# Kernel optimization log

Measured on AMD Instinct MI355X. Metric: run time of the kernel, lower is better.

The kernel has to match this reference:

```python
import jax, jax.numpy as jnp
import numpy as np


def _lstm(x, Wk, Wr, b, reverse, return_seq):
    # Keras LSTM with activation='relu', recurrent_activation='sigmoid'.
    # Wk: (F, 4H), Wr: (H, 4H), b: (4H). Gate order: i, f, c, o.
    if reverse:
        x = jnp.flip(x, 1)
    H = Wr.shape[0]
    xg = jnp.einsum('btf,fg->btg', x, Wk) + b  # (B, T, 4H)
    B = x.shape[0]

    def step(carry, g_t):
        h, c = carry
        g = g_t + h @ Wr
        i = jax.nn.sigmoid(g[:, :H])
        f = jax.nn.sigmoid(g[:, H:2 * H])
        cc = jax.nn.relu(g[:, 2 * H:3 * H])
        o = jax.nn.sigmoid(g[:, 3 * H:])
        c = f * c + i * cc
        h = o * jax.nn.relu(c)
        return (h, c), h

    init = (jnp.zeros((B, H), x.dtype), jnp.zeros((B, H), x.dtype))
    (h, _), hs = jax.lax.scan(step, init, jnp.swapaxes(xg, 0, 1))
    if return_seq:
        hs = jnp.swapaxes(hs, 0, 1)  # (B, T, H)
        if reverse:
            hs = jnp.flip(hs, 1)
        return hs
    return h


def setup_inputs() -> dict:
    key = jax.random.key(0)
    ks = jax.random.split(key, 24)
    B, LA, T, F = 256, 200, 512, 128
    s = 0.05
    d = {
        'inputA': jax.random.randint(ks[0], (B, LA), 0, 1000),
        'inputB': jax.random.normal(ks[1], (B, T, F), jnp.float32),
        'emb': jax.random.normal(ks[2], (1000, 3), jnp.float32) * s,
        'w1': jax.random.normal(ks[3], (600, 256), jnp.float32) * s,
        'b1': jnp.zeros((256,), jnp.float32),
        'w2': jax.random.normal(ks[4], (256, 128), jnp.float32) * s,
        'b2': jnp.zeros((128,), jnp.float32),
        'w3': jax.random.normal(ks[5], (128, 64), jnp.float32) * s,
        'b3': jnp.zeros((64,), jnp.float32),
        'k1f': jax.random.normal(ks[6], (128, 512), jnp.float32) * s,
        'r1f': jax.random.normal(ks[7], (128, 512), jnp.float32) * s,
        'bb1f': jnp.zeros((512,), jnp.float32),
        'k1b': jax.random.normal(ks[8], (128, 512), jnp.float32) * s,
        'r1b': jax.random.normal(ks[9], (128, 512), jnp.float32) * s,
        'bb1b': jnp.zeros((512,), jnp.float32),
        'k2f': jax.random.normal(ks[10], (256, 256), jnp.float32) * s,
        'r2f': jax.random.normal(ks[11], (64, 256), jnp.float32) * s,
        'bb2f': jnp.zeros((256,), jnp.float32),
        'k2b': jax.random.normal(ks[12], (256, 256), jnp.float32) * s,
        'r2b': jax.random.normal(ks[13], (64, 256), jnp.float32) * s,
        'bb2b': jnp.zeros((256,), jnp.float32),
        'wz1': jax.random.normal(ks[14], (192, 2), jnp.float32) * s,
        'bz1': jnp.zeros((2,), jnp.float32),
        'wz2': jax.random.normal(ks[15], (2, 1), jnp.float32) * s,
        'bz2': jnp.zeros((1,), jnp.float32),
        'wt1': jax.random.normal(ks[16], (192, 2), jnp.float32) * s,
        'bt1': jnp.zeros((2,), jnp.float32),
        'wt2': jax.random.normal(ks[17], (2, 1), jnp.float32) * s,
        'bt2': jnp.zeros((1,), jnp.float32),
    }
    return d


def reference(inputA, inputB, emb, w1, b1, w2, b2, w3, b3,
              k1f, r1f, bb1f, k1b, r1b, bb1b,
              k2f, r2f, bb2f, k2b, r2b, bb2b,
              wz1, bz1, wz2, bz2, wt1, bt1, wt2, bt2):
    B = inputA.shape[0]
    # Embedding branch
    x = emb[inputA]                       # (B, LA, 3)
    x = x.reshape(B, -1)                  # flatten -> (B, 600)
    x = jax.nn.relu(x @ w1 + b1)
    x = jax.nn.relu(x @ w2 + b2)
    x = jax.nn.relu(x @ w3 + b3)          # (B, 64)
    # BiLSTM branch
    y_f = _lstm(inputB, k1f, r1f, bb1f, reverse=False, return_seq=True)
    y_b = _lstm(inputB, k1b, r1b, bb1b, reverse=True, return_seq=True)
    y = jnp.concatenate([y_f, y_b], axis=-1)   # (B, T, 256)
    h_f = _lstm(y, k2f, r2f, bb2f, reverse=False, return_seq=False)
    h_b = _lstm(y, k2b, r2b, bb2b, reverse=True, return_seq=False)
    y = jnp.concatenate([h_f, h_b], axis=-1)    # (B, 128)
    combined = jnp.concatenate([x, y], axis=-1)  # (B, 192)
    z = jax.nn.relu(combined @ wz1 + bz1) @ wz2 + bz2
    t = jax.nn.relu(combined @ wt1 + bt1) @ wt2 + bt2
    return (z, t)
```

## Files before the change

kernel.cpp:

```cpp
#include <hip/hip_runtime.h>

typedef __attribute__((ext_vector_type(8))) short s8v;
typedef __attribute__((ext_vector_type(4))) short s4v;
typedef __attribute__((ext_vector_type(4))) float f4v;

#if __has_builtin(__builtin_amdgcn_exp2f)
#define EXP2(x) __builtin_amdgcn_exp2f(x)
#else
#define EXP2(x) exp2f(x)
#endif
#if __has_builtin(__builtin_amdgcn_rcpf)
#define RCP(x) __builtin_amdgcn_rcpf(x)
#else
#define RCP(x) (1.0f/(x))
#endif

#define LOG2E 1.4426950408889634f

__device__ __forceinline__ short f2bf(float f) {
    union { float f; unsigned u; } x; x.f = f;
    unsigned r = (x.u + 0x7FFFu + ((x.u >> 16) & 1u)) >> 16;
    return (short)r;
}
__device__ __forceinline__ float bf2f(short s) {
    union { unsigned u; float f; } x; x.u = ((unsigned)(unsigned short)s) << 16;
    return x.f;
}
__device__ __forceinline__ void lds_barrier() {
    asm volatile("s_waitcnt lgkmcnt(0)\n\ts_barrier" ::: "memory");
}

__global__ __launch_bounds__(256) void prep_embed_kernel(
        const float* __restrict__ k1f, const float* __restrict__ r1f,
        const float* __restrict__ k1b, const float* __restrict__ r1b,
        const float* __restrict__ k2f, const float* __restrict__ r2f,
        const float* __restrict__ k2b, const float* __restrict__ r2b,
        short* __restrict__ WB1, short* __restrict__ WB2,
        const int* __restrict__ inputA, const float* __restrict__ emb,
        const float* __restrict__ w1, const float* __restrict__ b1,
        const float* __restrict__ w2, const float* __restrict__ b2,
        const float* __restrict__ w3, const float* __restrict__ b3,
        float* __restrict__ xe) {
    if (blockIdx.x < 1024) {
        int idx = blockIdx.x * 256 + threadIdx.x;
        if (idx < 262144) {
            int j = idx & 7, l = (idx >> 3) & 63, c = (idx >> 9) & 7, n = (idx >> 12) & 31, d = (idx >> 17) & 1;
            int coln = n * 16 + (l & 15);
            int k = c * 32 + ((l >> 4) * 8) + j;
            const float* Wk = d ? k1b : k1f;
            const float* Wr = d ? r1b : r1f;
            float v = (c < 4) ? Wk[k * 512 + coln] : Wr[(k - 128) * 512 + coln];
            float sc = ((n >> 3) == 2) ? 1.0f : -LOG2E;
            WB1[idx] = f2bf(v * sc);
        }
        if (idx < 163840) {
            int d = idx / 81920, r0 = idx % 81920;
            int n = r0 / 5120, r1 = r0 % 5120;
            int c = r1 / 512, li = r1 % 512;
            int l = li >> 3, j = li & 7;
            int coln = n * 16 + (l & 15);
            int k = c * 32 + ((l >> 4) * 8) + j;
            const float* Wk = d ? k2b : k2f;
            const float* Wr = d ? r2b : r2f;
            float v = (k < 256) ? Wk[k * 256 + coln] : Wr[(k - 256) * 256 + coln];
            float sc = ((n >> 2) == 2) ? 1.0f : -LOG2E;
            WB2[idx] = f2bf(v * sc);
        }
        return;
    }
    __shared__ float row[600];
    __shared__ float h1[256];
    __shared__ float h2[128];
    int b = blockIdx.x - 1024, t = threadIdx.x;
    if (t < 200) {
        int idx = inputA[b * 200 + t];
        row[t * 3 + 0] = emb[idx * 3 + 0];
        row[t * 3 + 1] = emb[idx * 3 + 1];
        row[t * 3 + 2] = emb[idx * 3 + 2];
    }
    __syncthreads();
    float a = b1[t];
    for (int k = 0; k < 600; k++) a += row[k] * w1[k * 256 + t];
    h1[t] = fmaxf(a, 0.f);
    __syncthreads();
    if (t < 128) {
        float a2 = b2[t];
        for (int k = 0; k < 256; k++) a2 += h1[k] * w2[k * 128 + t];
        h2[t] = fmaxf(a2, 0.f);
    }
    __syncthreads();
    if (t < 64) {
        float a3 = b3[t];
        for (int k = 0; k < 128; k++) a3 += h2[k] * w3[k * 64 + t];
        xe[b * 64 + t] = fmaxf(a3, 0.f);
    }
}

__global__ __launch_bounds__(512, 2) void megastep(
        const float* __restrict__ x, const short* __restrict__ WB1, const short* __restrict__ WB2,
        const float* __restrict__ bb1f, const float* __restrict__ bb1b,
        const float* __restrict__ bb2f, const float* __restrict__ bb2b,
        short* __restrict__ yfr, short* __restrict__ xgA, short* __restrict__ xgB,
        short* __restrict__ ygA, short* __restrict__ ygB,
        float* __restrict__ c1st, short* __restrict__ h1st,
        float* __restrict__ c2st, short* __restrict__ h2st,
        float* __restrict__ h2o, int k, int TC, int NC) {
    __shared__ short hA[2048];
    __shared__ short hB[2048];
    __shared__ short stg[38912];
    const int tid = threadIdx.x, lane = tid & 63, w = tid >> 6;
    const int bid = blockIdx.x;
    const int tgn = TC >> 3;

    if (bid < 32) {
        const int cl = k - 1;
        if (cl < 0 || cl >= NC) return;
        const int t0 = cl * TC;
        const int first = (cl == 0);
        const int btile = bid & 15, dir = bid >> 4;
        const int col = lane & 15, q = lane >> 4, u = (w << 4) + col;
        const int sb = dir * 16 + btile;

        s8v wf[4][4];
#pragma unroll
        for (int ti = 0; ti < 4; ti++)
#pragma unroll
            for (int c = 0; c < 4; c++)
                wf[ti][c] = *(const s8v*)(WB1 + ((((dir * 32 + (w + 8 * ti)) * 8) + 4 + c) * 64 + lane) * 8);

        float cst[4], hl[4];
        if (first) {
#pragma unroll
            for (int r = 0; r < 4; r++) cst[r] = 0.f;
            for (int i = tid; i < 2048; i += 512) hA[i] = 0;
        } else {
            f4v cv = *(const f4v*)(c1st + ((size_t)sb * 8 + w) * 256 + lane * 4);
#pragma unroll
            for (int r = 0; r < 4; r++) cst[r] = cv[r];
            for (int i = tid; i < 2048; i += 512) hA[i] = h1st[sb * 2048 + i];
        }
        __syncthreads();

        const short* xgp = ((cl & 1) ? xgB : xgA) + (size_t)sb * TC * 8192 + w * 1024 + lane * 8;
        s8v pe0 = *(const s8v*)(xgp);
        s8v pe1 = *(const s8v*)(xgp + 512);
        s8v po0 = *(const s8v*)(xgp + 8192);
        s8v po1 = *(const s8v*)(xgp + 8192 + 512);

        const int hidx = (w >> 1) * 512 + ((u >> 3) & 3) * 128 + (u & 7);

        for (int s = 0; s < TC; s += 2) {
            {
                s8v ah[4];
#pragma unroll
                for (int cc = 0; cc < 4; cc++) ah[cc] = *(const s8v*)&hA[(cc * 64 + lane) * 8];
                if (w >= 4 && s > 0) {
                    int tp = t0 + s - 1;
                    if (dir) tp = 511 - tp;
                    s8v hv = (w == 4) ? ah[0] : (w == 5) ? ah[1] : (w == 6) ? ah[2] : ah[3];
                    *(s8v*)(yfr + (((size_t)(btile * 512 + tp) * 8) + dir * 4 + (w - 4)) * 512 + lane * 8) = hv;
                }
                f4v acc[4];
#pragma unroll
                for (int r = 0; r < 4; r++) {
                    acc[0][r] = bf2f(pe0[r]);
                    acc[1][r] = bf2f(pe0[4 + r]);
                    acc[2][r] = bf2f(pe1[r]);
                    acc[3][r] = bf2f(pe1[4 + r]);
                }
                {
                    const short* np = xgp + (size_t)(s + 2) * 8192;
                    pe0 = *(const s8v*)np;
                    pe1 = *(const s8v*)(np + 512);
                }
#pragma unroll
                for (int cc = 0; cc < 4; cc++)
#pragma unroll
                    for (int ti = 0; ti < 4; ti++)
                        acc[ti] = __builtin_amdgcn_mfma_f32_16x16x32_bf16(ah[cc], wf[ti][cc], acc[ti], 0, 0, 0);
#pragma unroll
                for (int r = 0; r < 4; r++) {
                    float iv = RCP(1.0f + EXP2(acc[0][r]));
                    float fv = RCP(1.0f + EXP2(acc[1][r]));
                    float ov = RCP(1.0f + EXP2(acc[3][r]));
                    float ccv = fmaxf(acc[2][r], 0.f);
                    cst[r] = fv * cst[r] + iv * ccv;
                    hl[r] = ov * fmaxf(cst[r], 0.f);
                }
#pragma unroll
                for (int r = 0; r < 4; r++)
                    hB[hidx + ((q * 4 + r) << 3)] = f2bf(hl[r]);
                lds_barrier();
            }
            {
                s8v ah[4];
#pragma unroll
                for (int cc = 0; cc < 4; cc++) ah[cc] = *(const s8v*)&hB[(cc * 64 + lane) * 8];
                if (w >= 4) {
                    int tp = t0 + s;
                    if (dir) tp = 511 - tp;
                    s8v hv = (w == 4) ? ah[0] : (w == 5) ? ah[1] : (w == 6) ? ah[2] : ah[3];
                    *(s8v*)(yfr + (((size_t)(btile * 512 + tp) * 8) + dir * 4 + (w - 4)) * 512 + lane * 8) = hv;
                }
                f4v acc[4];
#pragma unroll
                for (int r = 0; r < 4; r++) {
                    acc[0][r] = bf2f(po0[r]);
                    acc[1][r] = bf2f(po0[4 + r]);
                    acc[2][r] = bf2f(po1[r]);
                    acc[3][r] = bf2f(po1[4 + r]);
                }
                {
                    const short* np = xgp + (size_t)(s + 3) * 8192;
                    po0 = *(const s8v*)np;
                    po1 = *(const s8v*)(np + 512);
                }
#pragma unroll
                for (int cc = 0; cc < 4; cc++)
#pragma unroll
                    for (int ti = 0; ti < 4; ti++)
                        acc[ti] = __builtin_amdgcn_mfma_f32_16x16x32_bf16(ah[cc], wf[ti][cc], acc[ti], 0, 0, 0);
#pragma unroll
                for (int r = 0; r < 4; r++) {
                    float iv = RCP(1.0f + EXP2(acc[0][r]));
                    float fv = RCP(1.0f + EXP2(acc[1][r]));
                    float ov = RCP(1.0f + EXP2(acc[3][r]));
                    float ccv = fmaxf(acc[2][r], 0.f);
                    cst[r] = fv * cst[r] + iv * ccv;
                    hl[r] = ov * fmaxf(cst[r], 0.f);
                }
#pragma unroll
                for (int r = 0; r < 4; r++)
                    hA[hidx + ((q * 4 + r) << 3)] = f2bf(hl[r]);
                lds_barrier();
            }
        }
        if (w >= 4) {
            int tp = t0 + TC - 1;
            if (dir) tp = 511 - tp;
            s8v hv = *(const s8v*)&hA[((w - 4) * 64 + lane) * 8];
            *(s8v*)(yfr + (((size_t)(btile * 512 + tp) * 8) + dir * 4 + (w - 4)) * 512 + lane * 8) = hv;
        }
        f4v cv;
#pragma unroll
        for (int r = 0; r < 4; r++) cv[r] = cst[r];
        *(f4v*)(c1st + ((size_t)sb * 8 + w) * 256 + lane * 4) = cv;
        for (int i = tid; i < 2048; i += 512) h1st[sb * 2048 + i] = hA[i];
        return;
    }

    if (bid < 64) {
        const int c2 = k - 3;
        if (c2 < 0 || c2 >= NC) return;
        const int first = (c2 == 0), last = (c2 == NC - 1);
        const int btile = (bid - 32) & 15, dir = (bid - 32) >> 4;
        const int b0 = btile << 4;
        const int w4 = w & 3;
        const int col = lane & 15, q = lane >> 4, u = (w4 << 4) + col;
        const int sb = dir * 16 + btile;

        s8v wf[4][2];
#pragma unroll
        for (int ti = 0; ti < 4; ti++)
#pragma unroll
            for (int c = 0; c < 2; c++)
                wf[ti][c] = *(const s8v*)(WB2 + ((((dir * 16 + (w4 + 4 * ti)) * 10) + 8 + c) * 64 + lane) * 8);

        float cst[4], hl[4] = {0.f, 0.f, 0.f, 0.f};
        if (first) {
#pragma unroll
            for (int r = 0; r < 4; r++) cst[r] = 0.f;
            for (int i = tid; i < 1024; i += 512) hA[i] = 0;
        } else {
            f4v cv = *(const f4v*)(c2st + ((size_t)sb * 4 + w4) * 256 + lane * 4);
#pragma unroll
            for (int r = 0; r < 4; r++) cst[r] = cv[r];
            for (int i = tid; i < 1024; i += 512) hA[i] = h2st[sb * 1024 + i];
        }
        __syncthreads();

        const short* ygp = ((c2 & 1) ? ygB : ygA) + (size_t)sb * TC * 4096 + w4 * 1024 + lane * 8;
        s8v pe0, pe1, po0, po1;
        if (w < 4) {
            pe0 = *(const s8v*)(ygp);
            pe1 = *(const s8v*)(ygp + 512);
            po0 = *(const s8v*)(ygp + 4096);
            po1 = *(const s8v*)(ygp + 4096 + 512);
        }
        const int hidx = (w4 >> 1) * 512 + ((u >> 3) & 3) * 128 + (u & 7);

        for (int s = 0; s < TC; s += 2) {
            if (w < 4) {
                s8v ah[2];
#pragma unroll
                for (int cc = 0; cc < 2; cc++) ah[cc] = *(const s8v*)&hA[(cc * 64 + lane) * 8];
                f4v acc[4];
#pragma unroll
                for (int r = 0; r < 4; r++) {
                    acc[0][r] = bf2f(pe0[r]);
                    acc[1][r] = bf2f(pe0[4 + r]);
                    acc[2][r] = bf2f(pe1[r]);
                    acc[3][r] = bf2f(pe1[4 + r]);
                }
                {
                    const short* np = ygp + (size_t)(s + 2) * 4096;
                    pe0 = *(const s8v*)np;
                    pe1 = *(const s8v*)(np + 512);
                }
#pragma unroll
                for (int cc = 0; cc < 2; cc++)
#pragma unroll
                    for (int ti = 0; ti < 4; ti++)
                        acc[ti] = __builtin_amdgcn_mfma_f32_16x16x32_bf16(ah[cc], wf[ti][cc], acc[ti], 0, 0, 0);
#pragma unroll
                for (int r = 0; r < 4; r++) {
                    float iv = RCP(1.0f + EXP2(acc[0][r]));
                    float fv = RCP(1.0f + EXP2(acc[1][r]));
                    float ov = RCP(1.0f + EXP2(acc[3][r]));
                    float ccv = fmaxf(acc[2][r], 0.f);
                    cst[r] = fv * cst[r] + iv * ccv;
                    hl[r] = ov * fmaxf(cst[r], 0.f);
                }
#pragma unroll
                for (int r = 0; r < 4; r++)
                    hB[hidx + ((q * 4 + r) << 3)] = f2bf(hl[r]);
            }
            lds_barrier();
            if (w < 4) {
                s8v ah[2];
#pragma unroll
                for (int cc = 0; cc < 2; cc++) ah[cc] = *(const s8v*)&hB[(cc * 64 + lane) * 8];
                f4v acc[4];
#pragma unroll
                for (int r = 0; r < 4; r++) {
                    acc[0][r] = bf2f(po0[r]);
                    acc[1][r] = bf2f(po0[4 + r]);
                    acc[2][r] = bf2f(po1[r]);
                    acc[3][r] = bf2f(po1[4 + r]);
                }
                {
                    const short* np = ygp + (size_t)(s + 3) * 4096;
                    po0 = *(const s8v*)np;
                    po1 = *(const s8v*)(np + 512);
                }
#pragma unroll
                for (int cc = 0; cc < 2; cc++)
#pragma unroll
                    for (int ti = 0; ti < 4; ti++)
                        acc[ti] = __builtin_amdgcn_mfma_f32_16x16x32_bf16(ah[cc], wf[ti][cc], acc[ti], 0, 0, 0);
#pragma unroll
                for (int r = 0; r < 4; r++) {
                    float iv = RCP(1.0f + EXP2(acc[0][r]));
                    float fv = RCP(1.0f + EXP2(acc[1][r]));
                    float ov = RCP(1.0f + EXP2(acc[3][r]));
                    float ccv = fmaxf(acc[2][r], 0.f);
                    cst[r] = fv * cst[r] + iv * ccv;
                    hl[r] = ov * fmaxf(cst[r], 0.f);
                }
#pragma unroll
                for (int r = 0; r < 4; r++)
                    hA[hidx + ((q * 4 + r) << 3)] = f2bf(hl[r]);
            }
            lds_barrier();
        }
        if (w < 4) {
            f4v cv;
#pragma unroll
            for (int r = 0; r < 4; r++) cv[r] = cst[r];
            *(f4v*)(c2st + ((size_t)sb * 4 + w4) * 256 + lane * 4) = cv;
        }
        __syncthreads();
        for (int i = tid; i < 1024; i += 512) h2st[sb * 1024 + i] = hA[i];
        if (last && w < 4) {
#pragma unroll
            for (int r = 0; r < 4; r++)
                h2o[((dir * 256) + b0 + q * 4 + r) * 64 + u] = hl[r];
        }
        return;
    }

    if (bid < 64 + 4 * TC) {
        const int cg = k;
        if (cg >= NC) return;
        const int t0 = cg * TC;
        const int g = bid - 64;
        const int btile = g & 15;
        const int rest = g >> 4;
        const int tg = rest % tgn;
        const int dir = rest / tgn;
        const int b0 = btile << 4;
        short* xg_w = (cg & 1) ? xgB : xgA;
        {
            int tglob = t0 + tg * 8 + w;
            if (dir) tglob = 511 - tglob;
            const int half = lane >> 5;
            const int f0 = (lane & 31) * 4;
            const int cx = f0 >> 5, qq = (f0 >> 3) & 3, j0 = f0 & 7;
#pragma unroll
            for (int rr = 0; rr < 8; rr++) {
                const int m = rr * 2 + half;
                const float* xp = x + ((size_t)(b0 + m) * 512 + tglob) * 128 + f0;
                f4v v4 = *(const f4v*)xp;
                const int slot = (qq << 4) | ((m ^ qq ^ (cx << 1)) & 15);
                s4v pk;
#pragma unroll
                for (int j = 0; j < 4; j++) pk[j] = f2bf(v4[j]);
                *(s4v*)&stg[(((w * 4 + cx) * 64 + slot) * 8) + j0] = pk;
            }
        }
        s8v wf[4][4];
#pragma unroll
        for (int ti = 0; ti < 4; ti++)
#pragma unroll
            for (int c = 0; c < 4; c++)
                wf[ti][c] = *(const s8v*)(WB1 + ((((dir * 32 + (w + 8 * ti)) * 8) + c) * 64 + lane) * 8);
        const float* bb = dir ? bb1b : bb1f;
        float bias[4];
#pragma unroll
        for (int ti = 0; ti < 4; ti++) {
            const int tile = w + 8 * ti;
            float sc = ((tile >> 3) == 2) ? 1.0f : -LOG2E;
            bias[ti] = sc * bb[tile * 16 + (lane & 15)];
        }
        __syncthreads();
        const size_t sb = dir * 16 + btile;
#pragma unroll 2
        for (int sl = 0; sl < 8; sl++) {
            s8v a[4];
#pragma unroll
            for (int c = 0; c < 4; c++) {
                const int slot = lane ^ (lane >> 4) ^ (c << 1);
                a[c] = *(const s8v*)&stg[((sl * 4 + c) * 64 + slot) * 8];
            }
            f4v acc[4];
#pragma unroll
            for (int ti = 0; ti < 4; ti++) { f4v z = {0.f, 0.f, 0.f, 0.f}; acc[ti] = z; }
#pragma unroll
            for (int c = 0; c < 4; c++)
#pragma unroll
                for (int ti = 0; ti < 4; ti++)
                    acc[ti] = __builtin_amdgcn_mfma_f32_16x16x32_bf16(a[c], wf[ti][c], acc[ti], 0, 0, 0);
            short* outp = xg_w + ((sb * TC + (size_t)(tg * 8 + sl)) * 8 + w) * 1024 + lane * 8;
#pragma unroll
            for (int p = 0; p < 2; p++) {
                s8v v;
#pragma unroll
                for (int j = 0; j < 4; j++) {
                    v[j]     = f2bf(acc[2 * p][j]     + bias[2 * p]);
                    v[4 + j] = f2bf(acc[2 * p + 1][j] + bias[2 * p + 1]);
                }
                *(s8v*)(outp + p * 512) = v;
            }
        }
        return;
    }

    {
        const int cg = k - 2;
        if (cg < 0 || cg >= NC) return;
        const int t0 = cg * TC;
        const int g = bid - 64 - 4 * TC;
        const int btile = g & 15;
        const int rest = g >> 4;
        const int tg = rest % tgn;
        const int dir = rest / tgn;
        short* yg_w = (cg & 1) ? ygB : ygA;
        const int w4 = w & 3, sh = (w >> 2) * 4;
        s8v wf[4][8];
#pragma unroll
        for (int ti = 0; ti < 4; ti++)
#pragma unroll
            for (int c = 0; c < 8; c++)
                wf[ti][c] = *(const s8v*)(WB2 + ((((dir * 16 + (w4 + 4 * ti)) * 10) + c) * 64 + lane) * 8);
        const float* bb = dir ? bb2b : bb2f;
        float bias[4];
#pragma unroll
        for (int ti = 0; ti < 4; ti++) {
            const int tile = w4 + 4 * ti;
            float sc = ((tile >> 2) == 2) ? 1.0f : -LOG2E;
            bias[ti] = sc * bb[tile * 16 + (lane & 15)];
        }
        const size_t sb = dir * 16 + btile;
#pragma unroll
        for (int si = 0; si < 4; si++) {
            const int sl = sh + si;
            int tglob = t0 + tg * 8 + sl;
            if (dir) tglob = 511 - tglob;
            s8v a[8];
#pragma unroll
            for (int c = 0; c < 8; c++)
                a[c] = *(const s8v*)(yfr + (((size_t)(btile * 512 + tglob) * 8) + c) * 512 + lane * 8);
            f4v acc[4];
#pragma unroll
            for (int ti = 0; ti < 4; ti++) { f4v z = {0.f, 0.f, 0.f, 0.f}; acc[ti] = z; }
#pragma unroll
            for (int c = 0; c < 8; c++)
#pragma unroll
                for (int ti = 0; ti < 4; ti++)
                    acc[ti] = __builtin_amdgcn_mfma_f32_16x16x32_bf16(a[c], wf[ti][c], acc[ti], 0, 0, 0);
            short* outp = yg_w + ((sb * TC + (size_t)(tg * 8 + sl)) * 4 + w4) * 1024 + lane * 8;
#pragma unroll
            for (int p = 0; p < 2; p++) {
                s8v v;
#pragma unroll
                for (int j = 0; j < 4; j++) {
                    v[j]     = f2bf(acc[2 * p][j]     + bias[2 * p]);
                    v[4 + j] = f2bf(acc[2 * p + 1][j] + bias[2 * p + 1]);
                }
                *(s8v*)(outp + p * 512) = v;
            }
        }
    }
}

__global__ void heads_kernel(const float* __restrict__ xe, const float* __restrict__ h2o,
                             const float* __restrict__ wz1, const float* __restrict__ bz1,
                             const float* __restrict__ wz2, const float* __restrict__ bz2,
                             const float* __restrict__ wt1, const float* __restrict__ bt1,
                             const float* __restrict__ wt2, const float* __restrict__ bt2,
                             float* __restrict__ out) {
    int b = threadIdx.x;
    float cz0 = bz1[0], cz1 = bz1[1], ct0 = bt1[0], ct1 = bt1[1];
    for (int k = 0; k < 192; k++) {
        float v = (k < 64) ? xe[b * 64 + k]
                : (k < 128) ? h2o[b * 64 + (k - 64)]
                            : h2o[(256 + b) * 64 + (k - 128)];
        cz0 += v * wz1[k * 2 + 0];
        cz1 += v * wz1[k * 2 + 1];
        ct0 += v * wt1[k * 2 + 0];
        ct1 += v * wt1[k * 2 + 1];
    }
    cz0 = fmaxf(cz0, 0.f); cz1 = fmaxf(cz1, 0.f);
    ct0 = fmaxf(ct0, 0.f); ct1 = fmaxf(ct1, 0.f);
    out[b] = cz0 * wz2[0] + cz1 * wz2[1] + bz2[0];
    out[256 + b] = ct0 * wt2[0] + ct1 * wt2[1] + bt2[0];
}

extern "C" void kernel_launch(void* const* d_in, const int* in_sizes, int n_in,
                              void* d_out, int out_size, void* d_ws, size_t ws_size,
                              hipStream_t stream) {
    const int*   inputA = (const int*)d_in[0];
    const float* inputB = (const float*)d_in[1];
    const float* emb = (const float*)d_in[2];
    const float* w1  = (const float*)d_in[3];
    const float* b1  = (const float*)d_in[4];
    const float* w2  = (const float*)d_in[5];
    const float* b2  = (const float*)d_in[6];
    const float* w3  = (const float*)d_in[7];
    const float* b3  = (const float*)d_in[8];
    const float* k1f = (const float*)d_in[9];
    const float* r1f = (const float*)d_in[10];
    const float* bb1f= (const float*)d_in[11];
    const float* k1b = (const float*)d_in[12];
    const float* r1b = (const float*)d_in[13];
    const float* bb1b= (const float*)d_in[14];
    const float* k2f = (const float*)d_in[15];
    const float* r2f = (const float*)d_in[16];
    const float* bb2f= (const float*)d_in[17];
    const float* k2b = (const float*)d_in[18];
    const float* r2b = (const float*)d_in[19];
    const float* bb2b= (const float*)d_in[20];
    const float* wz1 = (const float*)d_in[21];
    const float* bz1 = (const float*)d_in[22];
    const float* wz2 = (const float*)d_in[23];
    const float* bz2 = (const float*)d_in[24];
    const float* wt1 = (const float*)d_in[25];
    const float* bt1 = (const float*)d_in[26];
    const float* wt2 = (const float*)d_in[27];
    const float* bt2 = (const float*)d_in[28];

    char* ws = (char*)d_ws;
    short* WB1  = (short*)(ws);
    short* WB2  = (short*)(ws + 524288);
    float* xe   = (float*)(ws + 851968);
    float* h2o  = (float*)(ws + 917504);
    float* c1st = (float*)(ws + 1048576);
    short* h1st = (short*)(ws + 1310720);
    float* c2st = (float*)(ws + 1441792);
    short* h2st = (short*)(ws + 1572864);
    short* yfr  = (short*)(ws + 2097152);
    float* out  = (float*)d_out;

    int TC = 32;
    if (69206016ull + 2ull * 64 * 524288 + 2ull * 64 * 262144 + 65536 <= ws_size) TC = 64;
    const int NC = 512 / TC;
    short* xgA = (short*)(ws + 69206016);
    short* xgB = xgA + (size_t)TC * 262144;
    short* ygA = xgB + (size_t)TC * 262144;
    short* ygB = ygA + (size_t)TC * 131072;
    const int grid = 64 + 8 * TC;

    prep_embed_kernel<<<1280, 256, 0, stream>>>(k1f, r1f, k1b, r1b, k2f, r2f, k2b, r2b,
                                                WB1, WB2, inputA, emb, w1, b1, w2, b2, w3, b3, xe);
    for (int k = 0; k < NC + 3; k++) {
        megastep<<<grid, 512, 0, stream>>>(inputB, WB1, WB2, bb1f, bb1b, bb2f, bb2b,
                                           yfr, xgA, xgB, ygA, ygB,
                                           c1st, h1st, c2st, h2st, h2o, k, TC, NC);
    }
    heads_kernel<<<1, 256, 0, stream>>>(xe, h2o, wz1, bz1, wz2, bz2, wt1, bt1, wt2, bt2, out);
}
```

Before: 673.4 us.

## Fuse layer-2 input projection into recurrent block via LDS ring, drop yg buffers

```diff
diff --git a/kernel.cpp b/kernel.cpp
--- a/kernel.cpp
+++ b/kernel.cpp
@@ -3,6 +3,7 @@
 typedef __attribute__((ext_vector_type(8))) short s8v;
 typedef __attribute__((ext_vector_type(4))) short s4v;
 typedef __attribute__((ext_vector_type(4))) float f4v;
+typedef __attribute__((ext_vector_type(4))) unsigned u4v;
 
 #if __has_builtin(__builtin_amdgcn_exp2f)
 #define EXP2(x) __builtin_amdgcn_exp2f(x)
@@ -22,9 +23,16 @@
     unsigned r = (x.u + 0x7FFFu + ((x.u >> 16) & 1u)) >> 16;
     return (short)r;
 }
-__device__ __forceinline__ float bf2f(short s) {
-    union { unsigned u; float f; } x; x.u = ((unsigned)(unsigned short)s) << 16;
-    return x.f;
+__device__ __forceinline__ float bflo(unsigned u) {
+    union { unsigned u; float f; } x; x.u = u << 16; return x.f;
+}
+__device__ __forceinline__ float bfhi(unsigned u) {
+    union { unsigned u; float f; } x; x.u = u & 0xffff0000u; return x.f;
+}
+__device__ __forceinline__ unsigned cvt_pk_bf16(float lo, float hi) {
+    unsigned r;
+    asm("v_cvt_pk_bf16_f32 %0, %1, %2" : "=v"(r) : "v"(lo), "v"(hi));
+    return r;
 }
 __device__ __forceinline__ void lds_barrier() {
     asm volatile("s_waitcnt lgkmcnt(0)\n\ts_barrier" ::: "memory");
@@ -101,13 +109,12 @@
         const float* __restrict__ bb1f, const float* __restrict__ bb1b,
         const float* __restrict__ bb2f, const float* __restrict__ bb2b,
         short* __restrict__ yfr, short* __restrict__ xgA, short* __restrict__ xgB,
-        short* __restrict__ ygA, short* __restrict__ ygB,
         float* __restrict__ c1st, short* __restrict__ h1st,
         float* __restrict__ c2st, short* __restrict__ h2st,
         float* __restrict__ h2o, int k, int TC, int NC) {
     __shared__ short hA[2048];
     __shared__ short hB[2048];
-    __shared__ short stg[38912];
+    __shared__ __align__(16) short stg[38912];
     const int tid = threadIdx.x, lane = tid & 63, w = tid >> 6;
     const int bid = blockIdx.x;
     const int tgn = TC >> 3;
@@ -128,7 +135,7 @@
             for (int c = 0; c < 4; c++)
                 wf[ti][c] = *(const s8v*)(WB1 + ((((dir * 32 + (w + 8 * ti)) * 8) + 4 + c) * 64 + lane) * 8);
 
-        float cst[4], hl[4];
+        float cst[4];
         if (first) {
 #pragma unroll
             for (int r = 0; r < 4; r++) cst[r] = 0.f;
@@ -142,10 +149,10 @@
         __syncthreads();
 
         const short* xgp = ((cl & 1) ? xgB : xgA) + (size_t)sb * TC * 8192 + w * 1024 + lane * 8;
-        s8v pe0 = *(const s8v*)(xgp);
-        s8v pe1 = *(const s8v*)(xgp + 512);
-        s8v po0 = *(const s8v*)(xgp + 8192);
-        s8v po1 = *(const s8v*)(xgp + 8192 + 512);
+        u4v pe0 = *(const u4v*)(xgp);
+        u4v pe1 = *(const u4v*)(xgp + 512);
+        u4v po0 = *(const u4v*)(xgp + 8192);
+        u4v po1 = *(const u4v*)(xgp + 8192 + 512);
 
         const int hidx = (w >> 1) * 512 + ((u >> 3) & 3) * 128 + (u & 7);
 
@@ -161,35 +168,37 @@
                     *(s8v*)(yfr + (((size_t)(btile * 512 + tp) * 8) + dir * 4 + (w - 4)) * 512 + lane * 8) = hv;
                 }
                 f4v acc[4];
-#pragma unroll
-                for (int r = 0; r < 4; r++) {
-                    acc[0][r] = bf2f(pe0[r]);
-                    acc[1][r] = bf2f(pe0[4 + r]);
-                    acc[2][r] = bf2f(pe1[r]);
-                    acc[3][r] = bf2f(pe1[4 + r]);
-                }
+                acc[0][0] = bflo(pe0[0]); acc[0][1] = bfhi(pe0[0]); acc[0][2] = bflo(pe0[1]); acc[0][3] = bfhi(pe0[1]);
+                acc[1][0] = bflo(pe0[2]); acc[1][1] = bfhi(pe0[2]); acc[1][2] = bflo(pe0[3]); acc[1][3] = bfhi(pe0[3]);
+                acc[2][0] = bflo(pe1[0]); acc[2][1] = bfhi(pe1[0]); acc[2][2] = bflo(pe1[1]); acc[2][3] = bfhi(pe1[1]);
+                acc[3][0] = bflo(pe1[2]); acc[3][1] = bfhi(pe1[2]); acc[3][2] = bflo(pe1[3]); acc[3][3] = bfhi(pe1[3]);
                 {
                     const short* np = xgp + (size_t)(s + 2) * 8192;
-                    pe0 = *(const s8v*)np;
-                    pe1 = *(const s8v*)(np + 512);
+                    pe0 = *(const u4v*)np;
+                    pe1 = *(const u4v*)(np + 512);
                 }
 #pragma unroll
                 for (int cc = 0; cc < 4; cc++)
 #pragma unroll
                     for (int ti = 0; ti < 4; ti++)
                         acc[ti] = __builtin_amdgcn_mfma_f32_16x16x32_bf16(ah[cc], wf[ti][cc], acc[ti], 0, 0, 0);
+                float hv_[4];
 #pragma unroll
                 for (int r = 0; r < 4; r++) {
-                    float iv = RCP(1.0f + EXP2(acc[0][r]));
-                    float fv = RCP(1.0f + EXP2(acc[1][r]));
-                    float ov = RCP(1.0f + EXP2(acc[3][r]));
-                    float ccv = fmaxf(acc[2][r], 0.f);
-                    cst[r] = fv * cst[r] + iv * ccv;
-                    hl[r] = ov * fmaxf(cst[r], 0.f);
-                }
-#pragma unroll
-                for (int r = 0; r < 4; r++)
-                    hB[hidx + ((q * 4 + r) << 3)] = f2bf(hl[r]);
+                    float Ei = EXP2(acc[0][r]);
+                    float Ef = EXP2(acc[1][r]);
+                    float Eo = EXP2(acc[3][r]);
+                    float rv = fmaxf(acc[2][r], 0.f);
+                    float di = 1.f + Ei, df = 1.f + Ef;
+                    float cn = fmaf(cst[r], di, rv * df) * RCP(di * df);
+                    cst[r] = cn;
+                    hv_[r] = fmaxf(cn, 0.f) * RCP(1.f + Eo);
+                }
+                unsigned p01 = cvt_pk_bf16(hv_[0], hv_[1]);
+                unsigned p23 = cvt_pk_bf16(hv_[2], hv_[3]);
+                short* hb = &hB[hidx + (q << 5)];
+                hb[0]  = (short)p01;  hb[8]  = (short)(p01 >> 16);
+                hb[16] = (short)p23;  hb[24] = (short)(p23 >> 16);
                 lds_barrier();
             }
             {
@@ -203,35 +212,37 @@
                     *(s8v*)(yfr + (((size_t)(btile * 512 + tp) * 8) + dir * 4 + (w - 4)) * 512 + lane * 8) = hv;
                 }
                 f4v acc[4];
-#pragma unroll
-                for (int r = 0; r < 4; r++) {
-                    acc[0][r] = bf2f(po0[r]);
-                    acc[1][r] = bf2f(po0[4 + r]);
-                    acc[2][r] = bf2f(po1[r]);
-                    acc[3][r] = bf2f(po1[4 + r]);
-                }
+                acc[0][0] = bflo(po0[0]); acc[0][1] = bfhi(po0[0]); acc[0][2] = bflo(po0[1]); acc[0][3] = bfhi(po0[1]);
+                acc[1][0] = bflo(po0[2]); acc[1][1] = bfhi(po0[2]); acc[1][2] = bflo(po0[3]); acc[1][3] = bfhi(po0[3]);
+                acc[2][0] = bflo(po1[0]); acc[2][1] = bfhi(po1[0]); acc[2][2] = bflo(po1[1]); acc[2][3] = bfhi(po1[1]);
+                acc[3][0] = bflo(po1[2]); acc[3][1] = bfhi(po1[2]); acc[3][2] = bflo(po1[3]); acc[3][3] = bfhi(po1[3]);
                 {
                     const short* np = xgp + (size_t)(s + 3) * 8192;
-                    po0 = *(const s8v*)np;
-                    po1 = *(const s8v*)(np + 512);
+                    po0 = *(const u4v*)np;
+                    po1 = *(const u4v*)(np + 512);
                 }
 #pragma unroll
                 for (int cc = 0; cc < 4; cc++)
 #pragma unroll
                     for (int ti = 0; ti < 4; ti++)
                         acc[ti] = __builtin_amdgcn_mfma_f32_16x16x32_bf16(ah[cc], wf[ti][cc], acc[ti], 0, 0, 0);
+                float hv_[4];
 #pragma unroll
                 for (int r = 0; r < 4; r++) {
-                    float iv = RCP(1.0f + EXP2(acc[0][r]));
-                    float fv = RCP(1.0f + EXP2(acc[1][r]));
-                    float ov = RCP(1.0f + EXP2(acc[3][r]));
-                    float ccv = fmaxf(acc[2][r], 0.f);
-                    cst[r] = fv * cst[r] + iv * ccv;
-                    hl[r] = ov * fmaxf(cst[r], 0.f);
-                }
-#pragma unroll
-                for (int r = 0; r < 4; r++)
-                    hA[hidx + ((q * 4 + r) << 3)] = f2bf(hl[r]);
+                    float Ei = EXP2(acc[0][r]);
+                    float Ef = EXP2(acc[1][r]);
+                    float Eo = EXP2(acc[3][r]);
+                    float rv = fmaxf(acc[2][r], 0.f);
+                    float di = 1.f + Ei, df = 1.f + Ef;
+                    float cn = fmaf(cst[r], di, rv * df) * RCP(di * df);
+                    cst[r] = cn;
+                    hv_[r] = fmaxf(cn, 0.f) * RCP(1.f + Eo);
+                }
+                unsigned p01 = cvt_pk_bf16(hv_[0], hv_[1]);
+                unsigned p23 = cvt_pk_bf16(hv_[2], hv_[3]);
+                short* hb = &hA[hidx + (q << 5)];
+                hb[0]  = (short)p01;  hb[8]  = (short)(p01 >> 16);
+                hb[16] = (short)p23;  hb[24] = (short)(p23 >> 16);
                 lds_barrier();
             }
         }
@@ -250,7 +261,7 @@
     }
 
     if (bid < 64) {
-        const int c2 = k - 3;
+        const int c2 = k - 2;
         if (c2 < 0 || c2 >= NC) return;
         const int first = (c2 == 0), last = (c2 == NC - 1);
         const int btile = (bid - 32) & 15, dir = (bid - 32) >> 4;
@@ -258,13 +269,8 @@
         const int w4 = w & 3;
         const int col = lane & 15, q = lane >> 4, u = (w4 << 4) + col;
         const int sb = dir * 16 + btile;
-
-        s8v wf[4][2];
-#pragma unroll
-        for (int ti = 0; ti < 4; ti++)
-#pragma unroll
-            for (int c = 0; c < 2; c++)
-                wf[ti][c] = *(const s8v*)(WB2 + ((((dir * 16 + (w4 + 4 * ti)) * 10) + 8 + c) * 64 + lane) * 8);
+        const int t0 = c2 * TC;
+        float* ring = (float*)stg;
 
         float cst[4], hl[4] = {0.f, 0.f, 0.f, 0.f};
         if (first) {
@@ -279,95 +285,179 @@
         }
         __syncthreads();
 
-        const short* ygp = ((c2 & 1) ? ygB : ygA) + (size_t)sb * TC * 4096 + w4 * 1024 + lane * 8;
-        s8v pe0, pe1, po0, po1;
+        const int hidx = (w4 >> 1) * 512 + ((u >> 3) & 3) * 128 + (u & 7);
+
         if (w < 4) {
-            pe0 = *(const s8v*)(ygp);
-            pe1 = *(const s8v*)(ygp + 512);
-            po0 = *(const s8v*)(ygp + 4096);
-            po1 = *(const s8v*)(ygp + 4096 + 512);
-        }
-        const int hidx = (w4 >> 1) * 512 + ((u >> 3) & 3) * 128 + (u & 7);
-
-        for (int s = 0; s < TC; s += 2) {
-            if (w < 4) {
-                s8v ah[2];
-#pragma unroll
-                for (int cc = 0; cc < 2; cc++) ah[cc] = *(const s8v*)&hA[(cc * 64 + lane) * 8];
-                f4v acc[4];
-#pragma unroll
-                for (int r = 0; r < 4; r++) {
-                    acc[0][r] = bf2f(pe0[r]);
-                    acc[1][r] = bf2f(pe0[4 + r]);
-                    acc[2][r] = bf2f(pe1[r]);
-                    acc[3][r] = bf2f(pe1[4 + r]);
-                }
+            s8v wr_[4][2];
+#pragma unroll
+            for (int ti = 0; ti < 4; ti++)
+#pragma unroll
+                for (int cc = 0; cc < 2; cc++)
+                    wr_[ti][cc] = *(const s8v*)(WB2 + ((((dir * 16 + (w4 + 4 * ti)) * 10) + 8 + cc) * 64 + lane) * 8);
+            lds_barrier();
+            for (int s = 0; s < TC; s += 2) {
                 {
-                    const short* np = ygp + (size_t)(s + 2) * 4096;
-                    pe0 = *(const s8v*)np;
-                    pe1 = *(const s8v*)(np + 512);
-                }
-#pragma unroll
-                for (int cc = 0; cc < 2; cc++)
+                    s8v ah[2];
+#pragma unroll
+                    for (int cc = 0; cc < 2; cc++) ah[cc] = *(const s8v*)&hA[(cc * 64 + lane) * 8];
+                    f4v acc[4];
+                    const int slot = s & 3;
 #pragma unroll
                     for (int ti = 0; ti < 4; ti++)
-                        acc[ti] = __builtin_amdgcn_mfma_f32_16x16x32_bf16(ah[cc], wf[ti][cc], acc[ti], 0, 0, 0);
-#pragma unroll
-                for (int r = 0; r < 4; r++) {
-                    float iv = RCP(1.0f + EXP2(acc[0][r]));
-                    float fv = RCP(1.0f + EXP2(acc[1][r]));
-                    float ov = RCP(1.0f + EXP2(acc[3][r]));
-                    float ccv = fmaxf(acc[2][r], 0.f);
-                    cst[r] = fv * cst[r] + iv * ccv;
-                    hl[r] = ov * fmaxf(cst[r], 0.f);
-                }
-#pragma unroll
-                for (int r = 0; r < 4; r++)
-                    hB[hidx + ((q * 4 + r) << 3)] = f2bf(hl[r]);
-            }
-            lds_barrier();
-            if (w < 4) {
-                s8v ah[2];
-#pragma unroll
-                for (int cc = 0; cc < 2; cc++) ah[cc] = *(const s8v*)&hB[(cc * 64 + lane) * 8];
-                f4v acc[4];
-#pragma unroll
-                for (int r = 0; r < 4; r++) {
-                    acc[0][r] = bf2f(po0[r]);
-                    acc[1][r] = bf2f(po0[4 + r]);
-                    acc[2][r] = bf2f(po1[r]);
-                    acc[3][r] = bf2f(po1[4 + r]);
+                        acc[ti] = *(const f4v*)&ring[(((slot * 4 + w4) * 4 + ti) * 64 + lane) * 4];
+#pragma unroll
+                    for (int cc = 0; cc < 2; cc++)
+#pragma unroll
+                        for (int ti = 0; ti < 4; ti++)
+                            acc[ti] = __builtin_amdgcn_mfma_f32_16x16x32_bf16(ah[cc], wr_[ti][cc], acc[ti], 0, 0, 0);
+#pragma unroll
+                    for (int r = 0; r < 4; r++) {
+                        float Ei = EXP2(acc[0][r]);
+                        float Ef = EXP2(acc[1][r]);
+                        float Eo = EXP2(acc[3][r]);
+                        float rv = fmaxf(acc[2][r], 0.f);
+                        float di = 1.f + Ei, df = 1.f + Ef;
+                        float cn = fmaf(cst[r], di, rv * df) * RCP(di * df);
+                        cst[r] = cn;
+                        hl[r] = fmaxf(cn, 0.f) * RCP(1.f + Eo);
+                    }
+                    unsigned p01 = cvt_pk_bf16(hl[0], hl[1]);
+                    unsigned p23 = cvt_pk_bf16(hl[2], hl[3]);
+                    short* hb = &hB[hidx + (q << 5)];
+                    hb[0]  = (short)p01;  hb[8]  = (short)(p01 >> 16);
+                    hb[16] = (short)p23;  hb[24] = (short)(p23 >> 16);
+                    lds_barrier();
                 }
                 {
-                    const short* np = ygp + (size_t)(s + 3) * 4096;
-                    po0 = *(const s8v*)np;
-                    po1 = *(const s8v*)(np + 512);
-                }
-#pragma unroll
-                for (int cc = 0; cc < 2; cc++)
+                    s8v ah[2];
+#pragma unroll
+                    for (int cc = 0; cc < 2; cc++) ah[cc] = *(const s8v*)&hB[(cc * 64 + lane) * 8];
+                    f4v acc[4];
+                    const int slot = (s + 1) & 3;
 #pragma unroll
                     for (int ti = 0; ti < 4; ti++)
-                        acc[ti] = __builtin_amdgcn_mfma_f32_16x16x32_bf16(ah[cc], wf[ti][cc], acc[ti], 0, 0, 0);
-#pragma unroll
-                for (int r = 0; r < 4; r++) {
-                    float iv = RCP(1.0f + EXP2(acc[0][r]));
-                    float fv = RCP(1.0f + EXP2(acc[1][r]));
-                    float ov = RCP(1.0f + EXP2(acc[3][r]));
-                    float ccv = fmaxf(acc[2][r], 0.f);
-                    cst[r] = fv * cst[r] + iv * ccv;
-                    hl[r] = ov * fmaxf(cst[r], 0.f);
-                }
-#pragma unroll
-                for (int r = 0; r < 4; r++)
-                    hA[hidx + ((q * 4 + r) << 3)] = f2bf(hl[r]);
-            }
-            lds_barrier();
-        }
-        if (w < 4) {
+                        acc[ti] = *(const f4v*)&ring[(((slot * 4 + w4) * 4 + ti) * 64 + lane) * 4];
+#pragma unroll
+                    for (int cc = 0; cc < 2; cc++)
+#pragma unroll
+                        for (int ti = 0; ti < 4; ti++)
+                            acc[ti] = __builtin_amdgcn_mfma_f32_16x16x32_bf16(ah[cc], wr_[ti][cc], acc[ti], 0, 0, 0);
+#pragma unroll
+                    for (int r = 0; r < 4; r++) {
+                        float Ei = EXP2(acc[0][r]);
+                        float Ef = EXP2(acc[1][r]);
+                        float Eo = EXP2(acc[3][r]);
+                        float rv = fmaxf(acc[2][r], 0.f);
+                        float di = 1.f + Ei, df = 1.f + Ef;
+                        float cn = fmaf(cst[r], di, rv * df) * RCP(di * df);
+                        cst[r] = cn;
+                        hl[r] = fmaxf(cn, 0.f) * RCP(1.f + Eo);
+                    }
+                    unsigned p01 = cvt_pk_bf16(hl[0], hl[1]);
+                    unsigned p23 = cvt_pk_bf16(hl[2], hl[3]);
+                    short* hb = &hA[hidx + (q << 5)];
+                    hb[0]  = (short)p01;  hb[8]  = (short)(p01 >> 16);
+                    hb[16] = (short)p23;  hb[24] = (short)(p23 >> 16);
+                    lds_barrier();
+                }
+            }
             f4v cv;
 #pragma unroll
             for (int r = 0; r < 4; r++) cv[r] = cst[r];
             *(f4v*)(c2st + ((size_t)sb * 4 + w4) * 256 + lane * 4) = cv;
+        } else {
+            const int p4 = w - 4;
+            s8v wk[4][8];
+#pragma unroll
+            for (int ti = 0; ti < 4; ti++)
+#pragma unroll
+                for (int c = 0; c < 8; c++)
+                    wk[ti][c] = *(const s8v*)(WB2 + ((((dir * 16 + (p4 + 4 * ti)) * 10) + c) * 64 + lane) * 8);
+            const float* bb = dir ? bb2b : bb2f;
+            float bias[4];
+#pragma unroll
+            for (int ti = 0; ti < 4; ti++) {
+                const int tile = p4 + 4 * ti;
+                float sc = ((tile >> 2) == 2) ? 1.0f : -LOG2E;
+                bias[ti] = sc * bb[tile * 16 + (lane & 15)];
+            }
+            int tg0 = dir ? (511 - t0) : t0;
+            const short* yrd = yfr + ((size_t)(btile * 512 + tg0) * 8) * 512 + lane * 8;
+            const int ystep = dir ? -4096 : 4096;
+            s8v aE[8], aO[8];
+#pragma unroll
+            for (int pt = 0; pt < 2; pt++) {
+                s8v a[8];
+#pragma unroll
+                for (int c = 0; c < 8; c++) a[c] = *(const s8v*)(yrd + c * 512);
+                yrd += ystep;
+                f4v acc[4];
+#pragma unroll
+                for (int ti = 0; ti < 4; ti++) { f4v z = {bias[ti], bias[ti], bias[ti], bias[ti]}; acc[ti] = z; }
+#pragma unroll
+                for (int c = 0; c < 8; c++)
+#pragma unroll
+                    for (int ti = 0; ti < 4; ti++)
+                        acc[ti] = __builtin_amdgcn_mfma_f32_16x16x32_bf16(a[c], wk[ti][c], acc[ti], 0, 0, 0);
+#pragma unroll
+                for (int ti = 0; ti < 4; ti++)
+                    *(f4v*)&ring[(((pt * 4 + p4) * 4 + ti) * 64 + lane) * 4] = acc[ti];
+            }
+#pragma unroll
+            for (int c = 0; c < 8; c++) aE[c] = *(const s8v*)(yrd + c * 512);
+            yrd += ystep;
+#pragma unroll
+            for (int c = 0; c < 8; c++) aO[c] = *(const s8v*)(yrd + c * 512);
+            yrd += ystep;
+            lds_barrier();
+            for (int s = 0; s < TC; s += 2) {
+                {
+                    const int t = s + 2;
+                    if (t < TC) {
+                        f4v acc[4];
+#pragma unroll
+                        for (int ti = 0; ti < 4; ti++) { f4v z = {bias[ti], bias[ti], bias[ti], bias[ti]}; acc[ti] = z; }
+#pragma unroll
+                        for (int c = 0; c < 8; c++)
+#pragma unroll
+                            for (int ti = 0; ti < 4; ti++)
+                                acc[ti] = __builtin_amdgcn_mfma_f32_16x16x32_bf16(aE[c], wk[ti][c], acc[ti], 0, 0, 0);
+                        const int slot = t & 3;
+#pragma unroll
+                        for (int ti = 0; ti < 4; ti++)
+                            *(f4v*)&ring[(((slot * 4 + p4) * 4 + ti) * 64 + lane) * 4] = acc[ti];
+                    }
+                    if (s + 4 < TC) {
+#pragma unroll
+                        for (int c = 0; c < 8; c++) aE[c] = *(const s8v*)(yrd + c * 512);
+                        yrd += ystep;
+                    }
+                    lds_barrier();
+                }
+                {
+                    const int t = s + 3;
+                    if (t < TC) {
+                        f4v acc[4];
+#pragma unroll
+                        for (int ti = 0; ti < 4; ti++) { f4v z = {bias[ti], bias[ti], bias[ti], bias[ti]}; acc[ti] = z; }
+#pragma unroll
+                        for (int c = 0; c < 8; c++)
+#pragma unroll
+                            for (int ti = 0; ti < 4; ti++)
+                                acc[ti] = __builtin_amdgcn_mfma_f32_16x16x32_bf16(aO[c], wk[ti][c], acc[ti], 0, 0, 0);
+                        const int slot = t & 3;
+#pragma unroll
+                        for (int ti = 0; ti < 4; ti++)
+                            *(f4v*)&ring[(((slot * 4 + p4) * 4 + ti) * 64 + lane) * 4] = acc[ti];
+                    }
+                    if (s + 5 < TC) {
+#pragma unroll
+                        for (int c = 0; c < 8; c++) aO[c] = *(const s8v*)(yrd + c * 512);
+                        yrd += ystep;
+                    }
+                    lds_barrier();
+                }
+            }
         }
         __syncthreads();
         for (int i = tid; i < 1024; i += 512) h2st[sb * 1024 + i] = hA[i];
@@ -379,7 +469,7 @@
         return;
     }
 
-    if (bid < 64 + 4 * TC) {
+    {
         const int cg = k;
         if (cg >= NC) return;
         const int t0 = cg * TC;
@@ -390,11 +480,12 @@
         const int dir = rest / tgn;
         const int b0 = btile << 4;
         short* xg_w = (cg & 1) ? xgB : xgA;
+        const int lane_ = lane;
         {
             int tglob = t0 + tg * 8 + w;
             if (dir) tglob = 511 - tglob;
-            const int half = lane >> 5;
-            const int f0 = (lane & 31) * 4;
+            const int half = lane_ >> 5;
+            const int f0 = (lane_ & 31) * 4;
             const int cx = f0 >> 5, qq = (f0 >> 3) & 3, j0 = f0 & 7;
 #pragma unroll
             for (int rr = 0; rr < 8; rr++) {
@@ -441,64 +532,6 @@
                 for (int ti = 0; ti < 4; ti++)
                     acc[ti] = __builtin_amdgcn_mfma_f32_16x16x32_bf16(a[c], wf[ti][c], acc[ti], 0, 0, 0);
             short* outp = xg_w + ((sb * TC + (size_t)(tg * 8 + sl)) * 8 + w) * 1024 + lane * 8;
-#pragma unroll
-            for (int p = 0; p < 2; p++) {
-                s8v v;
-#pragma unroll
-                for (int j = 0; j < 4; j++) {
-                    v[j]     = f2bf(acc[2 * p][j]     + bias[2 * p]);
-                    v[4 + j] = f2bf(acc[2 * p + 1][j] + bias[2 * p + 1]);
-                }
-                *(s8v*)(outp + p * 512) = v;
-            }
-        }
-        return;
-    }
-
-    {
-        const int cg = k - 2;
-        if (cg < 0 || cg >= NC) return;
-        const int t0 = cg * TC;
-        const int g = bid - 64 - 4 * TC;
-        const int btile = g & 15;
-        const int rest = g >> 4;
-        const int tg = rest % tgn;
-        const int dir = rest / tgn;
-        short* yg_w = (cg & 1) ? ygB : ygA;
-        const int w4 = w & 3, sh = (w >> 2) * 4;
-        s8v wf[4][8];
-#pragma unroll
-        for (int ti = 0; ti < 4; ti++)
-#pragma unroll
-            for (int c = 0; c < 8; c++)
-                wf[ti][c] = *(const s8v*)(WB2 + ((((dir * 16 + (w4 + 4 * ti)) * 10) + c) * 64 + lane) * 8);
-        const float* bb = dir ? bb2b : bb2f;
-        float bias[4];
-#pragma unroll
-        for (int ti = 0; ti < 4; ti++) {
-            const int tile = w4 + 4 * ti;
-            float sc = ((tile >> 2) == 2) ? 1.0f : -LOG2E;
-            bias[ti] = sc * bb[tile * 16 + (lane & 15)];
-        }
-        const size_t sb = dir * 16 + btile;
-#pragma unroll
-        for (int si = 0; si < 4; si++) {
-            const int sl = sh + si;
-            int tglob = t0 + tg * 8 + sl;
-            if (dir) tglob = 511 - tglob;
-            s8v a[8];
-#pragma unroll
-            for (int c = 0; c < 8; c++)
-                a[c] = *(const s8v*)(yfr + (((size_t)(btile * 512 + tglob) * 8) + c) * 512 + lane * 8);
-            f4v acc[4];
-#pragma unroll
-            for (int ti = 0; ti < 4; ti++) { f4v z = {0.f, 0.f, 0.f, 0.f}; acc[ti] = z; }
-#pragma unroll
-            for (int c = 0; c < 8; c++)
-#pragma unroll
-                for (int ti = 0; ti < 4; ti++)
-                    acc[ti] = __builtin_amdgcn_mfma_f32_16x16x32_bf16(a[c], wf[ti][c], acc[ti], 0, 0, 0);
-            short* outp = yg_w + ((sb * TC + (size_t)(tg * 8 + sl)) * 4 + w4) * 1024 + lane * 8;
 #pragma unroll
             for (int p = 0; p < 2; p++) {
                 s8v v;
@@ -586,15 +619,13 @@
     const int NC = 512 / TC;
     short* xgA = (short*)(ws + 69206016);
     short* xgB = xgA + (size_t)TC * 262144;
-    short* ygA = xgB + (size_t)TC * 262144;
-    short* ygB = ygA + (size_t)TC * 131072;
-    const int grid = 64 + 8 * TC;
+    const int grid = 64 + 4 * TC;
 
     prep_embed_kernel<<<1280, 256, 0, stream>>>(k1f, r1f, k1b, r1b, k2f, r2f, k2b, r2b,
                                                 WB1, WB2, inputA, emb, w1, b1, w2, b2, w3, b3, xe);
-    for (int k = 0; k < NC + 3; k++) {
+    for (int k = 0; k < NC + 2; k++) {
         megastep<<<grid, 512, 0, stream>>>(inputB, WB1, WB2, bb1f, bb1b, bb2f, bb2b,
-                                           yfr, xgA, xgB, ygA, ygB,
+                                           yfr, xgA, xgB,
                                            c1st, h1st, c2st, h2st, h2o, k, TC, NC);
     }
     heads_kernel<<<1, 256, 0, stream>>>(xe, h2o, wz1, bz1, wz2, bz2, wt1, bt1, wt2, bt2, out);
```

New measurement: 686.8 us. No clear change (+2.0%).
